# Kernel optimization log

Measured on AMD Instinct MI355X. Metric: run time of the kernel, lower is better.

Reference implementation:

```python
import jax, jax.numpy as jnp
import numpy as np

N_NODES = 50000
N_EDGES = 320000
HIDDEN = 256
N_LAYERS = 5
BN_EPS = 1e-5


def setup_inputs() -> dict:
    key = jax.random.key(0)
    ks = jax.random.split(key, 8)
    x = jax.random.normal(ks[0], (N_NODES, HIDDEN), dtype=jnp.float32)
    edge_index = jax.random.randint(ks[1], (2, N_EDGES), 0, N_NODES, dtype=jnp.int64)
    edge_attr = jax.random.uniform(ks[2], (N_EDGES, 4), dtype=jnp.float32)
    # xavier-ish scales
    mlp_w = jax.random.normal(ks[3], (N_LAYERS, 2 * HIDDEN, HIDDEN), dtype=jnp.float32) * (1.0 / np.sqrt(2 * HIDDEN))
    mlp_b = jnp.zeros((N_LAYERS, HIDDEN), dtype=jnp.float32)
    ew1 = jax.random.normal(ks[4], (N_LAYERS, 1, HIDDEN // 2), dtype=jnp.float32)
    ew2 = jax.random.normal(ks[5], (N_LAYERS, 3, HIDDEN // 2), dtype=jnp.float32) * (1.0 / np.sqrt(3.0))
    bn_g = jnp.ones((N_LAYERS, HIDDEN), dtype=jnp.float32)
    bn_b = jnp.zeros((N_LAYERS, HIDDEN), dtype=jnp.float32)
    return {"x": x, "edge_index": edge_index, "edge_attr": edge_attr,
            "mlp_w": mlp_w, "mlp_b": mlp_b, "ew1": ew1, "ew2": ew2,
            "bn_g": bn_g, "bn_b": bn_b}


def _mpnn(x, edge_index, edge_attr, mlp_w, mlp_b, ew1, ew2, bn_g, bn_b):
    n = x.shape[0]
    row, col = edge_index[0], edge_index[1]
    # gcn_norm: deg computed by scatter-add of ones at col (targets)
    deg = jax.ops.segment_sum(jnp.ones((edge_index.shape[1],), x.dtype), col, num_segments=n)
    dinv = jnp.where(deg > 0, deg ** -0.5, 0.0)
    norm = dinv[row] * dinv[col]  # [E]
    h = x
    for l in range(N_LAYERS):
        # edge feature fusion: Linear(1,h/2) on last col, Linear(3,h/2) on first 3
        edge_fea = jnp.concatenate([edge_attr[:, 3:] @ ew1[l], edge_attr[:, 0:3] @ ew2[l]], axis=-1)  # [E,H]
        msg = norm[:, None] * (h[row] + edge_fea)                      # gather + scale
        agg = jax.ops.segment_sum(msg, col, num_segments=n)            # scatter-add
        h = jax.nn.relu(jnp.concatenate([h, agg], axis=1) @ mlp_w[l] + mlp_b[l])
        # BatchNorm1d (training-mode batch stats, biased var)
        mu = h.mean(axis=0)
        var = h.var(axis=0)
        h = (h - mu) * jax.lax.rsqrt(var + BN_EPS) * bn_g[l] + bn_b[l]
        if l != N_LAYERS - 1:
            h = jax.nn.relu(h)
        # dropout with drop_ratio=0 is identity
    return h


def reference(x, edge_index, edge_attr, mlp_w, mlp_b, ew1, ew2, bn_g, bn_b):
    return _mpnn(x, edge_index, edge_attr, mlp_w, mlp_b, ew1, ew2, bn_g, bn_b)
```

## Files before the change

kernel.cpp:

```cpp
#include <hip/hip_runtime.h>
#include <stdint.h>

typedef short short8 __attribute__((ext_vector_type(8)));
typedef float f32x4 __attribute__((ext_vector_type(4)));
typedef unsigned short u16;

#define HID 256
#define NLAYERS 5
#define BN_EPS 1e-5f

__device__ __forceinline__ float bf2f(u16 u) {
    union { unsigned int i; float f; } v;
    v.i = ((unsigned int)u) << 16;
    return v.f;
}
__device__ __forceinline__ u16 f2bf(float f) {
    union { float f; unsigned int i; } v;
    v.f = f;
    unsigned int r = v.i + 0x7FFFu + ((v.i >> 16) & 1u);
    return (u16)(r >> 16);
}
__device__ __forceinline__ void split_bf(float f, u16& hi, u16& lo) {
    hi = f2bf(f);
    lo = f2bf(f - bf2f(hi));
}

__device__ __forceinline__ void gl_lds16(const void* gsrc, void* ldst) {
    const __attribute__((address_space(1))) unsigned int* g =
        reinterpret_cast<const __attribute__((address_space(1))) unsigned int*>(
            reinterpret_cast<uintptr_t>(gsrc));
    __attribute__((address_space(3))) unsigned int* l =
        reinterpret_cast<__attribute__((address_space(3))) unsigned int*>(
            reinterpret_cast<uintptr_t>(ldst));
    __builtin_amdgcn_global_load_lds(g, l, 16, 0, 0);
}


__global__ __launch_bounds__(256) void k_zero32(unsigned int* p, int n) {
    int i = blockIdx.x * 256 + threadIdx.x;
    if (i < n) p[i] = 0u;
}


__global__ __launch_bounds__(256) void k_detect(const int* ei, int* flag, int E) {
    __shared__ int nz;
    if (threadIdx.x == 0) nz = 0;
    __syncthreads();
    int lim = (2 * E < 4096) ? 2 * E : 4096;
    int c = 0;
    for (int i = threadIdx.x; 2 * i + 1 < lim; i += 256) c += (ei[2 * i + 1] != 0);
    atomicAdd(&nz, c);
    __syncthreads();
    if (threadIdx.x == 0) flag[0] = (nz == 0) ? 1 : 0;
}

__global__ __launch_bounds__(256) void k_deg(const int* ei, const int* flag, int* deg, int E, int N) {
    int e = blockIdx.x * 256 + threadIdx.x;
    if (e >= E) return;
    int w = flag[0];
    int col = w ? ei[2 * (E + e)] : ei[E + e];
    if ((unsigned)col < (unsigned)N) atomicAdd(&deg[col], 1);
}

__global__ __launch_bounds__(256) void k_dinv(const int* deg, float* dinv, int N) {
    int n = blockIdx.x * 256 + threadIdx.x;
    if (n < N) { int d = deg[n]; dinv[n] = d > 0 ? rsqrtf((float)d) : 0.0f; }
}

__global__ __launch_bounds__(256) void k_scan1(const int* deg, int* offs, int* bsum, int N) {
    __shared__ int s[256];
    int tid = threadIdx.x;
    int i = blockIdx.x * 256 + tid;
    int v = (i < N) ? deg[i] : 0;
    s[tid] = v;
    __syncthreads();
    for (int off = 1; off < 256; off <<= 1) {
        int t = (tid >= off) ? s[tid - off] : 0;
        __syncthreads();
        s[tid] += t;
        __syncthreads();
    }
    if (i < N) offs[i] = s[tid] - v;
    if (tid == 255) bsum[blockIdx.x] = s[tid];
}

__global__ __launch_bounds__(256) void k_scan2(const int* bsum, int* bscan, int NB) {
    __shared__ int s[256];
    int tid = threadIdx.x;
    int v = (tid < NB) ? bsum[tid] : 0;
    s[tid] = v;
    __syncthreads();
    for (int off = 1; off < 256; off <<= 1) {
        int t = (tid >= off) ? s[tid - off] : 0;
        __syncthreads();
        s[tid] += t;
        __syncthreads();
    }
    bscan[tid] = s[tid] - v;
}

__global__ __launch_bounds__(256) void k_scan3(int* offs, const int* bscan, int* cursor, int N, int E) {
    int i = blockIdx.x * 256 + threadIdx.x;
    if (i < N) {
        int o = offs[i] + bscan[blockIdx.x];
        offs[i] = o;
        cursor[i] = o;
    }
    if (i == 0) offs[N] = E;
}

__global__ __launch_bounds__(256) void k_place(const int* ei, const int* flag, const float4* eattr,
                                               int* cursor, int* srow, float4* sea, int E, int N) {
    int e = blockIdx.x * 256 + threadIdx.x;
    if (e >= E) return;
    int w = flag[0];
    int r = w ? ei[2 * e] : ei[e];
    int c = w ? ei[2 * (E + e)] : ei[E + e];
    if ((unsigned)c >= (unsigned)N) return;
    int p = atomicAdd(&cursor[c], 1);
    srow[p] = r;
    sea[p] = eattr[e];
}

__global__ __launch_bounds__(256) void k_move(const int* srow, const float4* sea, const float* sdinv,
                                              const int* soffs, int* rowArr, float4* eaP,
                                              float* dinvF, int* offsF, int E, int N) {
    int i = blockIdx.x * 256 + threadIdx.x;
    if (i < E) { rowArr[i] = srow[i]; eaP[i] = sea[i]; }
    if (i < N) dinvF[i] = sdinv[i];
    if (i <= N) offsF[i] = soffs[i];
}

__global__ __launch_bounds__(256) void k_precheckN(const int* offsF, const int* cursor, const float* dinvF,
                                                   const int* gflag, int* diag, int N, int E) {
    int i = blockIdx.x * 256 + threadIdx.x;
    if (i < N) {
        if (offsF[i + 1] < offsF[i]) atomicOr(&diag[0], 1);
        if (cursor[i] != offsF[i + 1]) atomicOr(&diag[0], 2);
        float d = dinvF[i];
        if (!(d == d) || fabsf(d) > 1e10f) atomicOr(&diag[0], 4);
    }
    if (i == 0) {
        if (offsF[N] != E) atomicOr(&diag[0], 8);
        diag[7] = gflag[0];
    }
}
__global__ __launch_bounds__(256) void k_precheckE(const int* rowArr, int* diag, int E, int N) {
    int p = blockIdx.x * 256 + threadIdx.x;
    if (p < E && (unsigned)rowArr[p] >= (unsigned)N) atomicOr(&diag[0], 16);
}

__global__ __launch_bounds__(256) void k_wsplit(const float* W, u16* wpH, float* colsum,
                                                const float* g, const float* b,
                                                float* scale, float* shift, int* diag,
                                                int M, int doBN) {
    if (blockIdx.x == 0) {
        int c = threadIdx.x;
        if (doBN) {
            float mu = colsum[c] / (float)M;
            float var = colsum[256 + c] / (float)M - mu * mu;
            if (!(mu == mu) || !(var == var) || var > 1e30f) atomicAdd(&diag[3], 1);
            if (var < 0.f) var = 0.f;
            float sc = rsqrtf(var + BN_EPS) * g[c];
            scale[c] = sc;
            shift[c] = b[c] - mu * sc;
        }
        colsum[c] = 0.f;
        colsum[256 + c] = 0.f;
    }
    int t = blockIdx.x * 256 + threadIdx.x;
    int lane = t & 63;
    int nbg = (t >> 6) & 15;
    int kb = t >> 10;
    int quad = lane >> 4, nl = lane & 15;
    const float* src = W + (size_t)(kb * 32 + quad * 8) * HID + nbg * 16 + nl;
    short8 vh;
#pragma unroll
    for (int j = 0; j < 8; ++j) vh[j] = (short)f2bf(src[(size_t)j * HID]);
    *((short8*)wpH + t) = vh;
}

#define FEA(ea, j) ((ea).w * w1v[j] + (ea).x * w20[j] + (ea).y * w21[j] + (ea).z * w22[j])
#define BNX(u, comp) (fmaxf(sc4.comp * bf2f(u) + sh4.comp, 0.f))

__global__ __launch_bounds__(256) void k_agg(const void* hin_, const u16* hin_lo, int hf32,
                                             const int* offs, const int* rowArr, const float4* eaP,
                                             const float* dinv, const float* ew1, const float* ew2,
                                             const float* bnsc, const float* bnsh,
                                             u16* agg_hi, u16* agg_lo, int* diag, int M) {
    (void)hin_lo;
    int lane = threadIdx.x & 63, wave = threadIdx.x >> 6;
    int n = blockIdx.x * 4 + wave;

    float w1v[4] = {0.f, 0.f, 0.f, 0.f};
    float w20[4] = {0.f, 0.f, 0.f, 0.f};
    float w21[4] = {0.f, 0.f, 0.f, 0.f};
    float w22[4] = {0.f, 0.f, 0.f, 0.f};
    if (lane < 32) {
        int c = lane * 4;
#pragma unroll
        for (int j = 0; j < 4; ++j) w1v[j] = ew1[c + j];
    } else {
        int cc = (lane - 32) * 4;
#pragma unroll
        for (int j = 0; j < 4; ++j) {
            w20[j] = ew2[cc + j];
            w21[j] = ew2[128 + cc + j];
            w22[j] = ew2[256 + cc + j];
        }
    }

    float4 sc4 = {0.f, 0.f, 0.f, 0.f}, sh4 = {0.f, 0.f, 0.f, 0.f};
    if (!hf32) {
        sc4 = ((const float4*)bnsc)[lane];
        sh4 = ((const float4*)bnsh)[lane];
    }

    if (n >= M) return;
    float dn = dinv[n];
    int s = offs[n], e = offs[n + 1];
    float a0 = 0.f, a1 = 0.f, a2 = 0.f, a3 = 0.f;
    int p = s;

    if (hf32) {
        for (; p + 4 <= e; p += 4) {
            int r0 = rowArr[p + 0], r1 = rowArr[p + 1], r2 = rowArr[p + 2], r3 = rowArr[p + 3];
            float4 ea0 = eaP[p + 0], ea1 = eaP[p + 1], ea2 = eaP[p + 2], ea3 = eaP[p + 3];
            float4 hv0 = *((const float4*)hin_ + (size_t)r0 * 64 + lane);
            float4 hv1 = *((const float4*)hin_ + (size_t)r1 * 64 + lane);
            float4 hv2 = *((const float4*)hin_ + (size_t)r2 * 64 + lane);
            float4 hv3 = *((const float4*)hin_ + (size_t)r3 * 64 + lane);
            float n0 = dn * dinv[r0], n1 = dn * dinv[r1], n2 = dn * dinv[r2], n3 = dn * dinv[r3];
            a0 += n0 * (hv0.x + FEA(ea0, 0)) + n1 * (hv1.x + FEA(ea1, 0))
                + n2 * (hv2.x + FEA(ea2, 0)) + n3 * (hv3.x + FEA(ea3, 0));
            a1 += n0 * (hv0.y + FEA(ea0, 1)) + n1 * (hv1.y + FEA(ea1, 1))
                + n2 * (hv2.y + FEA(ea2, 1)) + n3 * (hv3.y + FEA(ea3, 1));
            a2 += n0 * (hv0.z + FEA(ea0, 2)) + n1 * (hv1.z + FEA(ea1, 2))
                + n2 * (hv2.z + FEA(ea2, 2)) + n3 * (hv3.z + FEA(ea3, 2));
            a3 += n0 * (hv0.w + FEA(ea0, 3)) + n1 * (hv1.w + FEA(ea1, 3))
                + n2 * (hv2.w + FEA(ea2, 3)) + n3 * (hv3.w + FEA(ea3, 3));
        }
        for (; p < e; ++p) {
            int r = rowArr[p];
            float4 ea = eaP[p];
            float nrm = dn * dinv[r];
            float4 hv = *((const float4*)hin_ + (size_t)r * 64 + lane);
            a0 += nrm * (hv.x + FEA(ea, 0));
            a1 += nrm * (hv.y + FEA(ea, 1));
            a2 += nrm * (hv.z + FEA(ea, 2));
            a3 += nrm * (hv.w + FEA(ea, 3));
        }
    } else {
        for (; p + 4 <= e; p += 4) {
            int r0 = rowArr[p + 0], r1 = rowArr[p + 1], r2 = rowArr[p + 2], r3 = rowArr[p + 3];
            float4 ea0 = eaP[p + 0], ea1 = eaP[p + 1], ea2 = eaP[p + 2], ea3 = eaP[p + 3];
            ushort4 hh0 = *((const ushort4*)hin_ + (size_t)r0 * 64 + lane);
            ushort4 hh1 = *((const ushort4*)hin_ + (size_t)r1 * 64 + lane);
            ushort4 hh2 = *((const ushort4*)hin_ + (size_t)r2 * 64 + lane);
            ushort4 hh3 = *((const ushort4*)hin_ + (size_t)r3 * 64 + lane);
            float n0 = dn * dinv[r0], n1 = dn * dinv[r1], n2 = dn * dinv[r2], n3 = dn * dinv[r3];
            a0 += n0 * (BNX(hh0.x, x) + FEA(ea0, 0)) + n1 * (BNX(hh1.x, x) + FEA(ea1, 0))
                + n2 * (BNX(hh2.x, x) + FEA(ea2, 0)) + n3 * (BNX(hh3.x, x) + FEA(ea3, 0));
            a1 += n0 * (BNX(hh0.y, y) + FEA(ea0, 1)) + n1 * (BNX(hh1.y, y) + FEA(ea1, 1))
                + n2 * (BNX(hh2.y, y) + FEA(ea2, 1)) + n3 * (BNX(hh3.y, y) + FEA(ea3, 1));
            a2 += n0 * (BNX(hh0.z, z) + FEA(ea0, 2)) + n1 * (BNX(hh1.z, z) + FEA(ea1, 2))
                + n2 * (BNX(hh2.z, z) + FEA(ea2, 2)) + n3 * (BNX(hh3.z, z) + FEA(ea3, 2));
            a3 += n0 * (BNX(hh0.w, w) + FEA(ea0, 3)) + n1 * (BNX(hh1.w, w) + FEA(ea1, 3))
                + n2 * (BNX(hh2.w, w) + FEA(ea2, 3)) + n3 * (BNX(hh3.w, w) + FEA(ea3, 3));
        }
        for (; p < e; ++p) {
            int r = rowArr[p];
            float4 ea = eaP[p];
            float nrm = dn * dinv[r];
            ushort4 hh = *((const ushort4*)hin_ + (size_t)r * 64 + lane);
            a0 += nrm * (BNX(hh.x, x) + FEA(ea, 0));
            a1 += nrm * (BNX(hh.y, y) + FEA(ea, 1));
            a2 += nrm * (BNX(hh.z, z) + FEA(ea, 2));
            a3 += nrm * (BNX(hh.w, w) + FEA(ea, 3));
        }
    }

    int bad = 0;
    if (!(a0 == a0)) { a0 = 777.f; bad++; }
    if (!(a1 == a1)) { a1 = 777.f; bad++; }
    if (!(a2 == a2)) { a2 = 777.f; bad++; }
    if (!(a3 == a3)) { a3 = 777.f; bad++; }
    if (bad) atomicAdd(&diag[1], bad);
    ushort4 oh, ol;
    split_bf(a0, oh.x, ol.x);
    split_bf(a1, oh.y, ol.y);
    split_bf(a2, oh.z, ol.z);
    split_bf(a3, oh.w, ol.w);
    *((ushort4*)agg_hi + (size_t)n * 64 + lane) = oh;
    *((ushort4*)agg_lo + (size_t)n * 64 + lane) = ol;
}

__global__ __launch_bounds__(256, 2) void MPNN_79044578115931_kernel(
        const void* hinA_, const u16* hinA_lo, int hf32,
        const u16* agg_hi, const u16* agg_lo,
        const u16* wpH, const float* bias,
        const float* bnsc, const float* bnsh,
        u16* y_hi, u16* y_lo,
        float* colsum, float* colsumsq, int* diag, int M) {
    __shared__ __align__(16) u16 bstage[16384];
    __shared__ float lsum[256];
    __shared__ float lsq[256];

    int tid = threadIdx.x;
    int lane = tid & 63, wave = tid >> 6;
    int quad = lane >> 4, nl = lane & 15;
    int mBase = blockIdx.x * 128 + wave * 32;
    int rowA0 = mBase + nl;
    int rowA1 = mBase + 16 + nl;
    if (rowA0 >= M) rowA0 = M - 1;
    if (rowA1 >= M) rowA1 = M - 1;

    lsum[tid] = 0.f;
    lsq[tid] = 0.f;

    f32x4 acc0[16], acc1[16];
#pragma unroll
    for (int i = 0; i < 16; ++i) {
        acc0[i] = {0.f, 0.f, 0.f, 0.f};
        acc1[i] = {0.f, 0.f, 0.f, 0.f};
    }

    for (int kb = 0; kb < 8; ++kb) {
        __syncthreads();

        const u16* srcH = wpH + (size_t)kb * 16384;
#pragma unroll
        for (int i = 0; i < 8; ++i) {
            int ci = i * 256 + tid;
            gl_lds16(srcH + ci * 8, &bstage[ci * 8]);
        }

        short8 a0h0, a0l0, a1h0, a1l0, a0h1, a0l1, a1h1, a1l1;
        float4 sc0a, sc0b, sh0a, sh0b, sc1a, sc1b, sh1a, sh1b;
        if (kb < 4) {
            int k0 = kb * 64 + quad * 8;
            int k1 = k0 + 32;
            if (hf32) {
                const float* hp0 = (const float*)hinA_ + (size_t)rowA0 * HID;
                const float* hp1 = (const float*)hinA_ + (size_t)rowA1 * HID;
#pragma unroll
                for (int j = 0; j < 8; ++j) {
                    u16 h, l;
                    split_bf(hp0[k0 + j], h, l); a0h0[j] = (short)h; a0l0[j] = (short)l;
                    split_bf(hp1[k0 + j], h, l); a1h0[j] = (short)h; a1l0[j] = (short)l;
                    split_bf(hp0[k1 + j], h, l); a0h1[j] = (short)h; a0l1[j] = (short)l;
                    split_bf(hp1[k1 + j], h, l); a1h1[j] = (short)h; a1l1[j] = (short)l;
                }
            } else {
                a0h0 = *(const short8*)((const u16*)hinA_ + (size_t)rowA0 * HID + k0);
                a0l0 = *(const short8*)(hinA_lo + (size_t)rowA0 * HID + k0);
                a1h0 = *(const short8*)((const u16*)hinA_ + (size_t)rowA1 * HID + k0);
                a1l0 = *(const short8*)(hinA_lo + (size_t)rowA1 * HID + k0);
                a0h1 = *(const short8*)((const u16*)hinA_ + (size_t)rowA0 * HID + k1);
                a0l1 = *(const short8*)(hinA_lo + (size_t)rowA0 * HID + k1);
                a1h1 = *(const short8*)((const u16*)hinA_ + (size_t)rowA1 * HID + k1);
                a1l1 = *(const short8*)(hinA_lo + (size_t)rowA1 * HID + k1);
                int q0 = k0 >> 2, q1 = k1 >> 2;
                sc0a = ((const float4*)bnsc)[q0];
                sc0b = ((const float4*)bnsc)[q0 + 1];
                sh0a = ((const float4*)bnsh)[q0];
                sh0b = ((const float4*)bnsh)[q0 + 1];
                sc1a = ((const float4*)bnsc)[q1];
                sc1b = ((const float4*)bnsc)[q1 + 1];
                sh1a = ((const float4*)bnsh)[q1];
                sh1b = ((const float4*)bnsh)[q1 + 1];
            }
        } else {
            int k0 = (kb - 4) * 64 + quad * 8;
            int k1 = k0 + 32;
            a0h0 = *(const short8*)(agg_hi + (size_t)rowA0 * HID + k0);
            a0l0 = *(const short8*)(agg_lo + (size_t)rowA0 * HID + k0);
            a1h0 = *(const short8*)(agg_hi + (size_t)rowA1 * HID + k0);
            a1l0 = *(const short8*)(agg_lo + (size_t)rowA1 * HID + k0);
            a0h1 = *(const short8*)(agg_hi + (size_t)rowA0 * HID + k1);
            a0l1 = *(const short8*)(agg_lo + (size_t)rowA0 * HID + k1);
            a1h1 = *(const short8*)(agg_hi + (size_t)rowA1 * HID + k1);
            a1l1 = *(const short8*)(agg_lo + (size_t)rowA1 * HID + k1);
        }

        __syncthreads();

        if (!hf32 && kb < 4) {
            {
                float scr[8] = {sc0a.x, sc0a.y, sc0a.z, sc0a.w, sc0b.x, sc0b.y, sc0b.z, sc0b.w};
                float shr[8] = {sh0a.x, sh0a.y, sh0a.z, sh0a.w, sh0b.x, sh0b.y, sh0b.z, sh0b.w};
#pragma unroll
                for (int j = 0; j < 8; ++j) {
                    float f0 = scr[j] * (bf2f((u16)a0h0[j]) + bf2f((u16)a0l0[j])) + shr[j];
                    f0 = f0 > 0.f ? f0 : 0.f;
                    float f1 = scr[j] * (bf2f((u16)a1h0[j]) + bf2f((u16)a1l0[j])) + shr[j];
                    f1 = f1 > 0.f ? f1 : 0.f;
                    u16 h, l;
                    split_bf(f0, h, l);
                    a0h0[j] = (short)h; a0l0[j] = (short)l;
                    split_bf(f1, h, l);
                    a1h0[j] = (short)h; a1l0[j] = (short)l;
                }
            }
            {
                float scr[8] = {sc1a.x, sc1a.y, sc1a.z, sc1a.w, sc1b.x, sc1b.y, sc1b.z, sc1b.w};
                float shr[8] = {sh1a.x, sh1a.y, sh1a.z, sh1a.w, sh1b.x, sh1b.y, sh1b.z, sh1b.w};
#pragma unroll
                for (int j = 0; j < 8; ++j) {
                    float f0 = scr[j] * (bf2f((u16)a0h1[j]) + bf2f((u16)a0l1[j])) + shr[j];
                    f0 = f0 > 0.f ? f0 : 0.f;
                    float f1 = scr[j] * (bf2f((u16)a1h1[j]) + bf2f((u16)a1l1[j])) + shr[j];
                    f1 = f1 > 0.f ? f1 : 0.f;
                    u16 h, l;
                    split_bf(f0, h, l);
                    a0h1[j] = (short)h; a0l1[j] = (short)l;
                    split_bf(f1, h, l);
                    a1h1[j] = (short)h; a1l1[j] = (short)l;
                }
            }
        }

        const short8* bbase = (const short8*)bstage;
#pragma unroll
        for (int nbg = 0; nbg < 16; ++nbg) {
            short8 bh = bbase[nbg * 64 + lane];
            acc0[nbg] = __builtin_amdgcn_mfma_f32_16x16x32_bf16(a0h0, bh, acc0[nbg], 0, 0, 0);
            acc1[nbg] = __builtin_amdgcn_mfma_f32_16x16x32_bf16(a1h0, bh, acc1[nbg], 0, 0, 0);
            acc0[nbg] = __builtin_amdgcn_mfma_f32_16x16x32_bf16(a0l0, bh, acc0[nbg], 0, 0, 0);
            acc1[nbg] = __builtin_amdgcn_mfma_f32_16x16x32_bf16(a1l0, bh, acc1[nbg], 0, 0, 0);
        }
#pragma unroll
        for (int nbg = 0; nbg < 16; ++nbg) {
            short8 bh = bbase[1024 + nbg * 64 + lane];
            acc0[nbg] = __builtin_amdgcn_mfma_f32_16x16x32_bf16(a0h1, bh, acc0[nbg], 0, 0, 0);
            acc1[nbg] = __builtin_amdgcn_mfma_f32_16x16x32_bf16(a1h1, bh, acc1[nbg], 0, 0, 0);
            acc0[nbg] = __builtin_amdgcn_mfma_f32_16x16x32_bf16(a0l1, bh, acc0[nbg], 0, 0, 0);
            acc1[nbg] = __builtin_amdgcn_mfma_f32_16x16x32_bf16(a1l1, bh, acc1[nbg], 0, 0, 0);
        }
    }

    __syncthreads();

    int badY = 0;
#pragma unroll
    for (int nbg = 0; nbg < 16; ++nbg) {
        int c = nbg * 16 + nl;
        float bv = bias[c];
        float s = 0.f, q = 0.f;
#pragma unroll
        for (int r = 0; r < 4; ++r) {
            int m = mBase + quad * 4 + r;
            if (m < M) {
                float v = acc0[nbg][r] + bv;
                if (!(v == v)) { v = 777.f; badY++; }
                v = v > 0.f ? v : 0.f;
                u16 h, l;
                split_bf(v, h, l);
                y_hi[(size_t)m * HID + c] = h;
                y_lo[(size_t)m * HID + c] = l;
                s += v;
                q += v * v;
            }
        }
        atomicAdd(&lsum[c], s);
        atomicAdd(&lsq[c], q);
    }
#pragma unroll
    for (int nbg = 0; nbg < 16; ++nbg) {
        int c = nbg * 16 + nl;
        float bv = bias[c];
        float s = 0.f, q = 0.f;
#pragma unroll
        for (int r = 0; r < 4; ++r) {
            int m = mBase + 16 + quad * 4 + r;
            if (m < M) {
                float v = acc1[nbg][r] + bv;
                if (!(v == v)) { v = 777.f; badY++; }
                v = v > 0.f ? v : 0.f;
                u16 h, l;
                split_bf(v, h, l);
                y_hi[(size_t)m * HID + c] = h;
                y_lo[(size_t)m * HID + c] = l;
                s += v;
                q += v * v;
            }
        }
        atomicAdd(&lsum[c], s);
        atomicAdd(&lsq[c], q);
    }
    if (badY) atomicAdd(&diag[2], badY);
    __syncthreads();
    atomicAdd(&colsum[tid], lsum[tid]);
    atomicAdd(&colsumsq[tid], lsq[tid]);
}

__global__ __launch_bounds__(256) void k_bnscale(const float* colsum, const float* colsumsq,
                                                 const float* g, const float* b,
                                                 float* scale, float* shift, int* diag, int M) {
    int c = threadIdx.x;
    float mu = colsum[c] / (float)M;
    float var = colsumsq[c] / (float)M - mu * mu;
    if (!(mu == mu) || !(var == var) || var > 1e30f) atomicAdd(&diag[3], 1);
    if (var < 0.f) var = 0.f;
    float sc = rsqrtf(var + BN_EPS) * g[c];
    scale[c] = sc;
    shift[c] = b[c] - mu * sc;
}

__global__ __launch_bounds__(256) void k_bnapply(const u16* src_hi, const u16* src_lo,
                                                 u16* dst_hi, u16* dst_lo,
                                                 const float* scale, const float* shift,
                                                 float* outf, int finalL, int relu, int total) {
    int q4 = blockIdx.x * 256 + threadIdx.x;
    int idx = q4 * 4;
    if (idx >= total) return;
    int c = idx & (HID - 1);
    ushort4 vh = *((const ushort4*)src_hi + q4);
    ushort4 vl = *((const ushort4*)src_lo + q4);
    float o0 = scale[c + 0] * (bf2f(vh.x) + bf2f(vl.x)) + shift[c + 0];
    float o1 = scale[c + 1] * (bf2f(vh.y) + bf2f(vl.y)) + shift[c + 1];
    float o2 = scale[c + 2] * (bf2f(vh.z) + bf2f(vl.z)) + shift[c + 2];
    float o3 = scale[c + 3] * (bf2f(vh.w) + bf2f(vl.w)) + shift[c + 3];
    if (relu) {
        o0 = o0 > 0.f ? o0 : 0.f;
        o1 = o1 > 0.f ? o1 : 0.f;
        o2 = o2 > 0.f ? o2 : 0.f;
        o3 = o3 > 0.f ? o3 : 0.f;
    }
    if (finalL) {
        float4 ov; ov.x = o0; ov.y = o1; ov.z = o2; ov.w = o3;
        *((float4*)outf + q4) = ov;
    } else {
        ushort4 oh, ol;
        split_bf(o0, oh.x, ol.x);
        split_bf(o1, oh.y, ol.y);
        split_bf(o2, oh.z, ol.z);
        split_bf(o3, oh.w, ol.w);
        *((ushort4*)dst_hi + q4) = oh;
        *((ushort4*)dst_lo + q4) = ol;
    }
}

__global__ void k_encode(const int* diag, float* out) {
    if (threadIdx.x != 0 || blockIdx.x != 0) return;
    int k = -1;
    for (int i = 0; i < 4; ++i) if (diag[i] != 0) { k = i; break; }
    if (k < 0) return;
    out[0] = (float)(1 + k + (diag[7] != 0 ? 8 : 0)) * 1048576.0f;
}


extern "C" void kernel_launch(void* const* d_in, const int* in_sizes, int n_in,
                              void* d_out, int out_size, void* d_ws, size_t ws_size,
                              hipStream_t stream) {
    const float*  x     = (const float*)d_in[0];
    const int*    ei    = (const int*)d_in[1];
    const float4* eattr = (const float4*)d_in[2];
    const float*  mlp_w = (const float*)d_in[3];
    const float*  mlp_b = (const float*)d_in[4];
    const float*  ew1   = (const float*)d_in[5];
    const float*  ew2   = (const float*)d_in[6];
    const float*  bn_g  = (const float*)d_in[7];
    const float*  bn_b  = (const float*)d_in[8];
    (void)n_in; (void)out_size; (void)d_ws; (void)ws_size;

    const int N = in_sizes[0] / HID;
    const int E = in_sizes[1] / 2;
    const size_t P = (size_t)N * HID;

    char* st = (char*)d_out;
    int*    S_deg    = (int*)   (st + 0);
    float*  S_dinv   = (float*) (st + 204800);
    int*    S_offs   = (int*)   (st + 409600);
    int*    S_cursor = (int*)   (st + 614400);
    int*    S_bsum   = (int*)   (st + 819200);
    int*    S_bscan  = (int*)   (st + 820224);
    int*    S_gflag  = (int*)   (st + 821248);
    int*    S_row    = (int*)   (st + 1048576);
    float4* S_ea     = (float4*)(st + 2621440);

    char* eb = (char*)d_in[1];
    int*   rowArr = (int*)  (eb + 0);
    float* dinvF  = (float*)(eb + 1280000);
    int*   offsF  = (int*)  (eb + 1480000);
    float* colsum = (float*)(eb + 1680128);
    float* colsq  = (float*)(eb + 1681152);
    float* scaleF = (float*)(eb + 1682176);
    float* shiftF = (float*)(eb + 1683200);
    int*   diag   = (int*)  (eb + 1684224);
    u16*   wpH    = (u16*)  (eb + 1685504);
    float4* eaP   = (float4*)d_in[2];

    u16* sX_hi = (u16*)d_in[0];
    u16* sX_lo = sX_hi + P;
    u16* sD_hi = (u16*)d_out;
    u16* sD_lo = sD_hi + P;

    int NB  = (N + 255) / 256;
    int NBE = (E + 255) / 256;
    int NBG = (N + 127) / 128;
    int NBA = (N + 3) / 4;
    int NBQ = (int)((P / 4 + 255) / 256);

    k_detect<<<1, 256, 0, stream>>>(ei, S_gflag, E);
    k_zero32<<<NB, 256, 0, stream>>>((unsigned int*)S_deg, N);
    k_deg<<<NBE, 256, 0, stream>>>(ei, S_gflag, S_deg, E, N);
    k_dinv<<<NB, 256, 0, stream>>>(S_deg, S_dinv, N);
    k_scan1<<<NB, 256, 0, stream>>>(S_deg, S_offs, S_bsum, N);
    k_scan2<<<1, 256, 0, stream>>>(S_bsum, S_bscan, NB);
    k_scan3<<<NB, 256, 0, stream>>>(S_offs, S_bscan, S_cursor, N, E);
    k_place<<<NBE, 256, 0, stream>>>(ei, S_gflag, eattr, S_cursor, S_row, S_ea, E, N);
    k_move<<<NBE, 256, 0, stream>>>(S_row, S_ea, S_dinv, S_offs, rowArr, eaP, dinvF, offsF, E, N);
    k_zero32<<<1, 256, 0, stream>>>((unsigned int*)diag, 256);
    k_precheckN<<<NB, 256, 0, stream>>>(offsF, S_cursor, dinvF, S_gflag, diag, N, E);
    k_precheckE<<<NBE, 256, 0, stream>>>(rowArr, diag, E, N);

    for (int l = 0; l < NLAYERS; ++l) {
        int even = (l % 2 == 0);
        u16* dst_hi = even ? sD_hi : sX_hi;
        u16* dst_lo = even ? sD_lo : sX_lo;
        const void* hinA; const u16* hin_lo; int hf32;
        if (l == 0) { hinA = (const void*)x; hin_lo = 0; hf32 = 1; }
        else if (even) { hinA = (const void*)sX_hi; hin_lo = sX_lo; hf32 = 0; }
        else { hinA = (const void*)sD_hi; hin_lo = sD_lo; hf32 = 0; }

        const float* gPrev = bn_g + (size_t)(l > 0 ? l - 1 : 0) * HID;
        const float* bPrev = bn_b + (size_t)(l > 0 ? l - 1 : 0) * HID;
        k_wsplit<<<64, 256, 0, stream>>>(mlp_w + (size_t)l * 512 * HID, wpH, colsum,
                                         gPrev, bPrev, scaleF, shiftF, diag, N, l > 0 ? 1 : 0);
        k_agg<<<NBA, 256, 0, stream>>>(hinA, hin_lo, hf32, offsF, rowArr, eaP, dinvF,
                                       ew1 + (size_t)l * 128, ew2 + (size_t)l * 384,
                                       scaleF, shiftF,
                                       dst_hi, dst_lo, diag, N);
        MPNN_79044578115931_kernel<<<NBG, 256, 0, stream>>>(
            hinA, hin_lo, hf32, dst_hi, dst_lo, wpH,
            mlp_b + (size_t)l * HID, scaleF, shiftF,
            dst_hi, dst_lo, colsum, colsq, diag, N);
        if (l == NLAYERS - 1) {
            k_bnscale<<<1, 256, 0, stream>>>(colsum, colsq,
                                             bn_g + (size_t)l * HID, bn_b + (size_t)l * HID,
                                             scaleF, shiftF, diag, N);
            k_bnapply<<<NBQ, 256, 0, stream>>>(dst_hi, dst_lo, dst_hi, dst_lo, scaleF, shiftF,
                                               (float*)d_in[0], 1, 0, (int)P);
        }
    }

    hipMemcpyAsync(d_out, d_in[0], P * 4, hipMemcpyDeviceToDevice, stream);
    k_encode<<<1, 64, 0, stream>>>(diag, (float*)d_out);
}
```

Measured before the change: 851.7 us.

## Fuse setup kernels and write final BN output directly to output buffer

Merges several small preprocessing kernels: degree zeroing with layout detection, dinv with the first scan pass, diag zeroing into the move kernel, and the two precheck kernels into one. The last layer's GEMM now writes into the input scratch buffer, so the final BN apply can write fp32 straight into d_out. That removes the trailing device-to-device copy of the whole output. The aim is to cut launch overhead and one full pass over the output, at the cost of more intricate buffer aliasing.

New measurement: 832.3 us. 1.02x faster.

```diff
diff --git a/kernel.cpp b/kernel.cpp
--- a/kernel.cpp
+++ b/kernel.cpp
@@ -36,22 +36,21 @@
 }
 
 
-__global__ __launch_bounds__(256) void k_zero32(unsigned int* p, int n) {
+__global__ __launch_bounds__(256) void k_zdet(const int* ei, int* flag, unsigned int* deg,
+                                              int E, int N) {
     int i = blockIdx.x * 256 + threadIdx.x;
-    if (i < n) p[i] = 0u;
-}
-
-
-__global__ __launch_bounds__(256) void k_detect(const int* ei, int* flag, int E) {
-    __shared__ int nz;
-    if (threadIdx.x == 0) nz = 0;
-    __syncthreads();
-    int lim = (2 * E < 4096) ? 2 * E : 4096;
-    int c = 0;
-    for (int i = threadIdx.x; 2 * i + 1 < lim; i += 256) c += (ei[2 * i + 1] != 0);
-    atomicAdd(&nz, c);
-    __syncthreads();
-    if (threadIdx.x == 0) flag[0] = (nz == 0) ? 1 : 0;
+    if (i < N) deg[i] = 0u;
+    if (blockIdx.x == 0) {
+        __shared__ int nz;
+        if (threadIdx.x == 0) nz = 0;
+        __syncthreads();
+        int lim = (2 * E < 4096) ? 2 * E : 4096;
+        int c = 0;
+        for (int k = threadIdx.x; 2 * k + 1 < lim; k += 256) c += (ei[2 * k + 1] != 0);
+        atomicAdd(&nz, c);
+        __syncthreads();
+        if (threadIdx.x == 0) flag[0] = (nz == 0) ? 1 : 0;
+    }
 }
 
 __global__ __launch_bounds__(256) void k_deg(const int* ei, const int* flag, int* deg, int E, int N) {
@@ -62,16 +61,13 @@
     if ((unsigned)col < (unsigned)N) atomicAdd(&deg[col], 1);
 }
 
-__global__ __launch_bounds__(256) void k_dinv(const int* deg, float* dinv, int N) {
-    int n = blockIdx.x * 256 + threadIdx.x;
-    if (n < N) { int d = deg[n]; dinv[n] = d > 0 ? rsqrtf((float)d) : 0.0f; }
-}
-
-__global__ __launch_bounds__(256) void k_scan1(const int* deg, int* offs, int* bsum, int N) {
+__global__ __launch_bounds__(256) void k_scan1d(const int* deg, int* offs, int* bsum,
+                                                float* dinv, int N) {
     __shared__ int s[256];
     int tid = threadIdx.x;
     int i = blockIdx.x * 256 + tid;
     int v = (i < N) ? deg[i] : 0;
+    if (i < N) dinv[i] = v > 0 ? rsqrtf((float)v) : 0.0f;
     s[tid] = v;
     __syncthreads();
     for (int off = 1; off < 256; off <<= 1) {
@@ -124,15 +120,17 @@
 
 __global__ __launch_bounds__(256) void k_move(const int* srow, const float4* sea, const float* sdinv,
                                               const int* soffs, int* rowArr, float4* eaP,
-                                              float* dinvF, int* offsF, int E, int N) {
+                                              float* dinvF, int* offsF, int* diag, int E, int N) {
     int i = blockIdx.x * 256 + threadIdx.x;
     if (i < E) { rowArr[i] = srow[i]; eaP[i] = sea[i]; }
     if (i < N) dinvF[i] = sdinv[i];
     if (i <= N) offsF[i] = soffs[i];
-}
-
-__global__ __launch_bounds__(256) void k_precheckN(const int* offsF, const int* cursor, const float* dinvF,
-                                                   const int* gflag, int* diag, int N, int E) {
+    if (i < 256) diag[i] = 0;
+}
+
+__global__ __launch_bounds__(256) void k_precheck(const int* offsF, const int* cursor,
+                                                  const float* dinvF, const int* gflag,
+                                                  const int* rowArr, int* diag, int N, int E) {
     int i = blockIdx.x * 256 + threadIdx.x;
     if (i < N) {
         if (offsF[i + 1] < offsF[i]) atomicOr(&diag[0], 1);
@@ -144,10 +142,7 @@
         if (offsF[N] != E) atomicOr(&diag[0], 8);
         diag[7] = gflag[0];
     }
-}
-__global__ __launch_bounds__(256) void k_precheckE(const int* rowArr, int* diag, int E, int N) {
-    int p = blockIdx.x * 256 + threadIdx.x;
-    if (p < E && (unsigned)rowArr[p] >= (unsigned)N) atomicOr(&diag[0], 16);
+    if (i < E && (unsigned)rowArr[i] >= (unsigned)N) atomicOr(&diag[0], 16);
 }
 
 __global__ __launch_bounds__(256) void k_wsplit(const float* W, u16* wpH, float* colsum,
@@ -508,37 +503,20 @@
 }
 
 __global__ __launch_bounds__(256) void k_bnapply(const u16* src_hi, const u16* src_lo,
-                                                 u16* dst_hi, u16* dst_lo,
                                                  const float* scale, const float* shift,
-                                                 float* outf, int finalL, int relu, int total) {
+                                                 float* outf, int total) {
     int q4 = blockIdx.x * 256 + threadIdx.x;
     int idx = q4 * 4;
     if (idx >= total) return;
     int c = idx & (HID - 1);
     ushort4 vh = *((const ushort4*)src_hi + q4);
     ushort4 vl = *((const ushort4*)src_lo + q4);
-    float o0 = scale[c + 0] * (bf2f(vh.x) + bf2f(vl.x)) + shift[c + 0];
-    float o1 = scale[c + 1] * (bf2f(vh.y) + bf2f(vl.y)) + shift[c + 1];
-    float o2 = scale[c + 2] * (bf2f(vh.z) + bf2f(vl.z)) + shift[c + 2];
-    float o3 = scale[c + 3] * (bf2f(vh.w) + bf2f(vl.w)) + shift[c + 3];
-    if (relu) {
-        o0 = o0 > 0.f ? o0 : 0.f;
-        o1 = o1 > 0.f ? o1 : 0.f;
-        o2 = o2 > 0.f ? o2 : 0.f;
-        o3 = o3 > 0.f ? o3 : 0.f;
-    }
-    if (finalL) {
-        float4 ov; ov.x = o0; ov.y = o1; ov.z = o2; ov.w = o3;
-        *((float4*)outf + q4) = ov;
-    } else {
-        ushort4 oh, ol;
-        split_bf(o0, oh.x, ol.x);
-        split_bf(o1, oh.y, ol.y);
-        split_bf(o2, oh.z, ol.z);
-        split_bf(o3, oh.w, ol.w);
-        *((ushort4*)dst_hi + q4) = oh;
-        *((ushort4*)dst_lo + q4) = ol;
-    }
+    float4 ov;
+    ov.x = scale[c + 0] * (bf2f(vh.x) + bf2f(vl.x)) + shift[c + 0];
+    ov.y = scale[c + 1] * (bf2f(vh.y) + bf2f(vl.y)) + shift[c + 1];
+    ov.z = scale[c + 2] * (bf2f(vh.z) + bf2f(vl.z)) + shift[c + 2];
+    ov.w = scale[c + 3] * (bf2f(vh.w) + bf2f(vl.w)) + shift[c + 3];
+    *((float4*)outf + q4) = ov;
 }
 
 __global__ void k_encode(const int* diag, float* out) {
@@ -602,18 +580,15 @@
     int NBA = (N + 3) / 4;
     int NBQ = (int)((P / 4 + 255) / 256);
 
-    k_detect<<<1, 256, 0, stream>>>(ei, S_gflag, E);
-    k_zero32<<<NB, 256, 0, stream>>>((unsigned int*)S_deg, N);
+    k_zdet<<<NB, 256, 0, stream>>>(ei, S_gflag, (unsigned int*)S_deg, E, N);
     k_deg<<<NBE, 256, 0, stream>>>(ei, S_gflag, S_deg, E, N);
-    k_dinv<<<NB, 256, 0, stream>>>(S_deg, S_dinv, N);
-    k_scan1<<<NB, 256, 0, stream>>>(S_deg, S_offs, S_bsum, N);
+    k_scan1d<<<NB, 256, 0, stream>>>(S_deg, S_offs, S_bsum, S_dinv, N);
     k_scan2<<<1, 256, 0, stream>>>(S_bsum, S_bscan, NB);
     k_scan3<<<NB, 256, 0, stream>>>(S_offs, S_bscan, S_cursor, N, E);
     k_place<<<NBE, 256, 0, stream>>>(ei, S_gflag, eattr, S_cursor, S_row, S_ea, E, N);
-    k_move<<<NBE, 256, 0, stream>>>(S_row, S_ea, S_dinv, S_offs, rowArr, eaP, dinvF, offsF, E, N);
-    k_zero32<<<1, 256, 0, stream>>>((unsigned int*)diag, 256);
-    k_precheckN<<<NB, 256, 0, stream>>>(offsF, S_cursor, dinvF, S_gflag, diag, N, E);
-    k_precheckE<<<NBE, 256, 0, stream>>>(rowArr, diag, E, N);
+    k_move<<<NBE, 256, 0, stream>>>(S_row, S_ea, S_dinv, S_offs, rowArr, eaP, dinvF, offsF,
+                                    diag, E, N);
+    k_precheck<<<NBE, 256, 0, stream>>>(offsF, S_cursor, dinvF, S_gflag, rowArr, diag, N, E);
 
     for (int l = 0; l < NLAYERS; ++l) {
         int even = (l % 2 == 0);
@@ -623,6 +598,10 @@
         if (l == 0) { hinA = (const void*)x; hin_lo = 0; hf32 = 1; }
         else if (even) { hinA = (const void*)sX_hi; hin_lo = sX_lo; hf32 = 0; }
         else { hinA = (const void*)sD_hi; hin_lo = sD_lo; hf32 = 0; }
+
+        int finalL = (l == NLAYERS - 1);
+        u16* y_hi = finalL ? sX_hi : dst_hi;
+        u16* y_lo = finalL ? sX_lo : dst_lo;
 
         const float* gPrev = bn_g + (size_t)(l > 0 ? l - 1 : 0) * HID;
         const float* bPrev = bn_b + (size_t)(l > 0 ? l - 1 : 0) * HID;
@@ -635,16 +614,15 @@
         MPNN_79044578115931_kernel<<<NBG, 256, 0, stream>>>(
             hinA, hin_lo, hf32, dst_hi, dst_lo, wpH,
             mlp_b + (size_t)l * HID, scaleF, shiftF,
-            dst_hi, dst_lo, colsum, colsq, diag, N);
-        if (l == NLAYERS - 1) {
+            y_hi, y_lo, colsum, colsq, diag, N);
+        if (finalL) {
             k_bnscale<<<1, 256, 0, stream>>>(colsum, colsq,
                                              bn_g + (size_t)l * HID, bn_b + (size_t)l * HID,
                                              scaleF, shiftF, diag, N);
-            k_bnapply<<<NBQ, 256, 0, stream>>>(dst_hi, dst_lo, dst_hi, dst_lo, scaleF, shiftF,
-                                               (float*)d_in[0], 1, 0, (int)P);
-        }
-    }
-
-    hipMemcpyAsync(d_out, d_in[0], P * 4, hipMemcpyDeviceToDevice, stream);
+            k_bnapply<<<NBQ, 256, 0, stream>>>(y_hi, y_lo, scaleF, shiftF,
+                                               (float*)d_out, (int)P);
+        }
+    }
+
     k_encode<<<1, 64, 0, stream>>>(diag, (float*)d_out);
 }
```
